# Performance work log

Hardware: AMD Instinct MI355X
Metric: run time of the kernel (lower is better)

## Reference

```python
import jax, jax.numpy as jnp
import numpy as np

B, H, W, C = 16, 64, 64, 256
DIM = 256

def setup_inputs() -> dict:
    key = jax.random.key(0)
    ks = jax.random.split(key, 9)
    s_in = 1.0 / np.sqrt(C)
    x = jax.random.normal(ks[0], (B, H, W, C), dtype=jnp.float32)
    Wq = jax.random.normal(ks[1], (C, DIM), dtype=jnp.float32) * s_in
    bq = jnp.zeros((DIM,), dtype=jnp.float32)
    Wk = jax.random.normal(ks[2], (C, DIM), dtype=jnp.float32) * s_in
    bk = jnp.zeros((DIM,), dtype=jnp.float32)
    Wv = jax.random.normal(ks[3], (C, DIM), dtype=jnp.float32) * s_in
    bv = jnp.zeros((DIM,), dtype=jnp.float32)
    # 'out' conv sees 1 input channel (after the channel reduce_sum)
    Wo = jax.random.normal(ks[4], (1, DIM), dtype=jnp.float32)
    bo = jnp.zeros((DIM,), dtype=jnp.float32)
    return {"x": x, "Wq": Wq, "bq": bq, "Wk": Wk, "bk": bk,
            "Wv": Wv, "bv": bv, "Wo": Wo, "bo": bo}

def reference(x, Wq, bq, Wk, bk, Wv, bv, Wo, bo):
    # 1x1 convs == channel GEMMs
    q = jnp.einsum('bhwc,cd->bhwd', x, Wq) + bq
    k = jnp.einsum('bhwc,cd->bhwd', x, Wk) + bk
    v = jnp.einsum('bhwc,cd->bhwd', x, Wv) + bv
    # channel-reduce score -> [B,H,W,1], softmax jointly over spatial axes
    score = jnp.sum(q * k, axis=-1, keepdims=True)
    attn = jax.nn.softmax(score, axis=(1, 2))
    # channel-reduce of v weighted by per-pixel attn -> [B,H,W,1]
    out = jnp.sum(v * attn, axis=-1, keepdims=True)
    # final 1x1 conv: 1 input channel -> DIM output channels
    return jnp.einsum('bhwc,cd->bhwd', out, Wo) + bo
```

## Files before the change

kernel.cpp:

```cpp
#include <hip/hip_runtime.h>


typedef __bf16 bf16_t;
typedef __attribute__((ext_vector_type(8))) __bf16 bf16x8;
typedef __attribute__((ext_vector_type(4))) __bf16 bf16x4;
typedef __attribute__((ext_vector_type(4))) float f32x4;

#define NBATCH 16
#define CCH    256
#define NPIX   65536
#define PPB    4096

#define MH_OFF    0u
#define ML_OFF    131072u
#define U_OFF     262144u
#define WV_OFF    263168u
#define SCL_OFF   264192u
#define SCORE_OFF 264448u
#define SV_OFF    526592u
#define BMAX_OFF  788736u
#define BSUM_OFF  788800u

__global__ __launch_bounds__(256) void prep_kernel(
    const float* __restrict__ Wq, const float* __restrict__ bq,
    const float* __restrict__ Wk, const float* __restrict__ bk,
    const float* __restrict__ Wv, const float* __restrict__ bv,
    bf16_t* __restrict__ Mh, bf16_t* __restrict__ Ml,
    float* __restrict__ u, float* __restrict__ wv, float* __restrict__ scl)
{
    const int t = threadIdx.x;
    if (blockIdx.x < 256) {
        const int c = blockIdx.x;
        __shared__ __align__(16) float wq_row[256];
        wq_row[t] = Wq[c * 256 + t];
        __syncthreads();
        const float4* wk4 = (const float4*)(Wk + t * 256);
        const float4* wq4 = (const float4*)wq_row;
        float acc = 0.f;
#pragma unroll 8
        for (int i = 0; i < 64; ++i) {
            float4 a = wq4[i], b = wk4[i];
            acc += a.x * b.x + a.y * b.y + a.z * b.z + a.w * b.w;
        }
        bf16_t h = (bf16_t)acc;
        float hf = (float)h;
        bf16_t l = (bf16_t)(acc - hf);
        Mh[c * 256 + t] = h;
        Ml[c * 256 + t] = l;
    } else {
        float uacc = 0.f, wvacc = 0.f;
        const float* wqr = Wq + t * 256;
        const float* wkr = Wk + t * 256;
        const float* wvr = Wv + t * 256;
#pragma unroll 4
        for (int d = 0; d < 256; ++d) {
            uacc += wqr[d] * bk[d] + wkr[d] * bq[d];
            wvacc += wvr[d];
        }
        u[t] = uacc;
        wv[t] = wvacc;
        __shared__ float r1[256], r2[256];
        r1[t] = bq[t] * bk[t];
        r2[t] = bv[t];
        __syncthreads();
        for (int s = 128; s > 0; s >>= 1) {
            if (t < s) { r1[t] += r1[t + s]; r2[t] += r2[t + s]; }
            __syncthreads();
        }
        if (t == 0) { scl[0] = r1[0]; scl[1] = r2[0]; }
    }
}

__global__ __launch_bounds__(256) void score_kernel(
    const float* __restrict__ x,
    const bf16_t* __restrict__ Mh, const bf16_t* __restrict__ Ml,
    const float* __restrict__ u, const float* __restrict__ wvp,
    const float* __restrict__ scl,
    float* __restrict__ score, float* __restrict__ svout)
{
    __shared__ __align__(16) bf16_t Ah[128][72];
    __shared__ __align__(16) bf16_t Al[128][72];
    __shared__ float redS[4][128];
    __shared__ float redV[4][128];

    const int t = threadIdx.x;
    const int lane = t & 63;
    const int wid = t >> 6;
    const int l15 = lane & 15;
    const int lg = lane >> 4;
    const int pix0 = blockIdx.x * 128;
    const int wcol0 = wid * 64;

    f32x4 acc[8][4];
#pragma unroll
    for (int i = 0; i < 8; ++i)
#pragma unroll
        for (int j = 0; j < 4; ++j)
            acc[i][j] = (f32x4){0.f, 0.f, 0.f, 0.f};

    for (int kc = 0; kc < 4; ++kc) {
        const int k0 = kc * 64;
        __syncthreads();
#pragma unroll
        for (int i = 0; i < 8; ++i) {
            int li = i * 256 + t;
            int r = li >> 4;
            int c4 = (li & 15) << 2;
            float4 xv = *(const float4*)(x + (size_t)(pix0 + r) * 256 + k0 + c4);
            bf16x4 hi, lo;
            hi[0] = (bf16_t)xv.x; hi[1] = (bf16_t)xv.y;
            hi[2] = (bf16_t)xv.z; hi[3] = (bf16_t)xv.w;
            lo[0] = (bf16_t)(xv.x - (float)hi[0]);
            lo[1] = (bf16_t)(xv.y - (float)hi[1]);
            lo[2] = (bf16_t)(xv.z - (float)hi[2]);
            lo[3] = (bf16_t)(xv.w - (float)hi[3]);
            *(bf16x4*)&Ah[r][c4] = hi;
            *(bf16x4*)&Al[r][c4] = lo;
        }
        __syncthreads();
#pragma unroll
        for (int seg = 0; seg < 3; ++seg) {
            const bf16_t* Bsrc = (seg == 2) ? Ml : Mh;
#pragma unroll
            for (int ks = 0; ks < 2; ++ks) {
                const int kk = ks * 32;
                bf16x8 af[8];
#pragma unroll
                for (int rf = 0; rf < 8; ++rf) {
                    const bf16_t* ap = (seg == 1) ? &Al[rf * 16 + l15][kk + lg * 8]
                                                  : &Ah[rf * 16 + l15][kk + lg * 8];
                    af[rf] = *(const bf16x8*)ap;
                }
                bf16x8 bfr[4];
#pragma unroll
                for (int cf = 0; cf < 4; ++cf) {
                    int col = wcol0 + cf * 16 + l15;
                    bfr[cf] = *(const bf16x8*)(Bsrc + (size_t)col * 256 + k0 + kk + lg * 8);
                }
#pragma unroll
                for (int rf = 0; rf < 8; ++rf)
#pragma unroll
                    for (int cf = 0; cf < 4; ++cf)
                        acc[rf][cf] = __builtin_amdgcn_mfma_f32_16x16x32_bf16(
                            af[rf], bfr[cf], acc[rf][cf], 0, 0, 0);
            }
        }
    }

    float uu[4], wvl[4];
#pragma unroll
    for (int cf = 0; cf < 4; ++cf) {
        uu[cf] = u[wcol0 + cf * 16 + l15];
        wvl[cf] = wvp[wcol0 + cf * 16 + l15];
    }
#pragma unroll
    for (int rf = 0; rf < 8; ++rf) {
#pragma unroll
        for (int r = 0; r < 4; ++r) {
            int row = rf * 16 + lg * 4 + r;
            const float* xr = x + (size_t)(pix0 + row) * 256 + wcol0 + l15;
            float s = 0.f, v = 0.f;
#pragma unroll
            for (int cf = 0; cf < 4; ++cf) {
                float xv = xr[cf * 16];
                s += xv * (acc[rf][cf][r] + uu[cf]);
                v += xv * wvl[cf];
            }
#pragma unroll
            for (int m = 1; m < 16; m <<= 1) {
                s += __shfl_xor(s, m, 64);
                v += __shfl_xor(v, m, 64);
            }
            if (l15 == 0) { redS[wid][row] = s; redV[wid][row] = v; }
        }
    }
    __syncthreads();
    if (t < 128) {
        float c0 = scl[0], bvs = scl[1];
        float s = redS[0][t] + redS[1][t] + redS[2][t] + redS[3][t] + c0;
        float v = redV[0][t] + redV[1][t] + redV[2][t] + redV[3][t] + bvs;
        score[pix0 + t] = s;
        svout[pix0 + t] = v;
    }
}

__global__ __launch_bounds__(256) void stats_kernel(
    const float* __restrict__ score,
    float* __restrict__ bmax, float* __restrict__ bsum)
{
    const int b = blockIdx.x, t = threadIdx.x;
    const float* s = score + b * PPB;
    __shared__ float red[256];
    float m = -1e30f;
    for (int i = t; i < PPB; i += 256) m = fmaxf(m, s[i]);
    red[t] = m;
    __syncthreads();
    for (int k = 128; k > 0; k >>= 1) {
        if (t < k) red[t] = fmaxf(red[t], red[t + k]);
        __syncthreads();
    }
    m = red[0];
    __syncthreads();
    float sum = 0.f;
    for (int i = t; i < PPB; i += 256) sum += __expf(s[i] - m);
    red[t] = sum;
    __syncthreads();
    for (int k = 128; k > 0; k >>= 1) {
        if (t < k) red[t] += red[t + k];
        __syncthreads();
    }
    if (t == 0) { bmax[b] = m; bsum[b] = red[0]; }
}

__global__ __launch_bounds__(256) void out_kernel(
    const float* __restrict__ score, const float* __restrict__ sv,
    const float* __restrict__ bmax, const float* __restrict__ bsum,
    const float* __restrict__ Wo, const float* __restrict__ bo,
    float* __restrict__ out)
{
    const int total = NPIX * 64;
    const int stride = gridDim.x * blockDim.x;
    for (int idx = blockIdx.x * blockDim.x + threadIdx.x; idx < total; idx += stride) {
        int p = idx >> 6;
        int c4 = (idx & 63) << 2;
        int b = p >> 12;
        float g = __expf(score[p] - bmax[b]) / bsum[b] * sv[p];
        float4 w = *(const float4*)(Wo + c4);
        float4 bb = *(const float4*)(bo + c4);
        float4 o = { g * w.x + bb.x, g * w.y + bb.y, g * w.z + bb.z, g * w.w + bb.w };
        *(float4*)(out + (size_t)p * 256 + c4) = o;
    }
}

extern "C" void kernel_launch(void* const* d_in, const int* in_sizes, int n_in,
                              void* d_out, int out_size, void* d_ws, size_t ws_size,
                              hipStream_t stream) {
    const float* x  = (const float*)d_in[0];
    const float* Wq = (const float*)d_in[1];
    const float* bq = (const float*)d_in[2];
    const float* Wk = (const float*)d_in[3];
    const float* bk = (const float*)d_in[4];
    const float* Wv = (const float*)d_in[5];
    const float* bv = (const float*)d_in[6];
    const float* Wo = (const float*)d_in[7];
    const float* bo = (const float*)d_in[8];
    float* out = (float*)d_out;
    char* ws = (char*)d_ws;

    bf16_t* Mh = (bf16_t*)(ws + MH_OFF);
    bf16_t* Ml = (bf16_t*)(ws + ML_OFF);
    float* u   = (float*)(ws + U_OFF);
    float* wv  = (float*)(ws + WV_OFF);
    float* scl = (float*)(ws + SCL_OFF);
    float* score = (float*)(ws + SCORE_OFF);
    float* sv    = (float*)(ws + SV_OFF);
    float* bmax  = (float*)(ws + BMAX_OFF);
    float* bsum  = (float*)(ws + BSUM_OFF);

    prep_kernel<<<dim3(257), dim3(256), 0, stream>>>(Wq, bq, Wk, bk, Wv, bv, Mh, Ml, u, wv, scl);
    score_kernel<<<dim3(NPIX / 128), dim3(256), 0, stream>>>(x, Mh, Ml, u, wv, scl, score, sv);
    stats_kernel<<<dim3(NBATCH), dim3(256), 0, stream>>>(score, bmax, bsum);
    out_kernel<<<dim3(2048), dim3(256), 0, stream>>>(score, sv, bmax, bsum, Wo, bo, out);
}
```

Measured before the change: 125.8 us.

## Stage full-K x tile in swizzled LDS, halve pixel tile, reuse LDS for epilogue

The score kernel now loads a whole 64-pixel by 256-channel x tile into LDS at once as bf16 hi/lo, using an XOR swizzle instead of padding, rather than looping over four K-chunks with a sync around each. It drops from 128 to 64 pixels per block, doubling the grid and cutting accumulators from 32 to 16 fragments to help fit two blocks per CU. The epilogue rebuilds x from hi+lo in LDS instead of re-reading x from global memory, and the reduction buffers share the same LDS. Each block now uses 64KB of LDS, which caps occupancy, and B fragments are reloaded from global for half as many rows, so weight reuse per load is lower.

```diff
diff --git a/kernel.cpp b/kernel.cpp
--- a/kernel.cpp
+++ b/kernel.cpp
@@ -7,7 +7,6 @@
 typedef __attribute__((ext_vector_type(4))) float f32x4;
 
 #define NBATCH 16
-#define CCH    256
 #define NPIX   65536
 #define PPB    4096
 
@@ -71,80 +70,94 @@
     }
 }
 
-__global__ __launch_bounds__(256) void score_kernel(
+__device__ __forceinline__ int swz(int row, int col) {
+    return row * 256 + (col ^ ((row & 7) << 3));
+}
+
+__global__ __launch_bounds__(256, 2) void score_kernel(
     const float* __restrict__ x,
     const bf16_t* __restrict__ Mh, const bf16_t* __restrict__ Ml,
     const float* __restrict__ u, const float* __restrict__ wvp,
     const float* __restrict__ scl,
     float* __restrict__ score, float* __restrict__ svout)
 {
-    __shared__ __align__(16) bf16_t Ah[128][72];
-    __shared__ __align__(16) bf16_t Al[128][72];
-    __shared__ float redS[4][128];
-    __shared__ float redV[4][128];
+    __shared__ __align__(16) char smem[65536];
+    bf16_t* Ah = (bf16_t*)smem;
+    bf16_t* Al = Ah + 16384;
+    float* redS = (float*)smem;
+    float* redV = redS + 256;
 
     const int t = threadIdx.x;
     const int lane = t & 63;
     const int wid = t >> 6;
     const int l15 = lane & 15;
     const int lg = lane >> 4;
-    const int pix0 = blockIdx.x * 128;
+    const int pix0 = blockIdx.x * 64;
     const int wcol0 = wid * 64;
 
-    f32x4 acc[8][4];
-#pragma unroll
-    for (int i = 0; i < 8; ++i)
+#pragma unroll
+    for (int i = 0; i < 16; ++i) {
+        int chunk = i * 256 + t;
+        int r = chunk >> 6;
+        int c4 = (chunk & 63) << 2;
+        float4 xv = *(const float4*)(x + (size_t)(pix0 + r) * 256 + c4);
+        bf16x4 hi, lo;
+        hi[0] = (bf16_t)xv.x; hi[1] = (bf16_t)xv.y;
+        hi[2] = (bf16_t)xv.z; hi[3] = (bf16_t)xv.w;
+        lo[0] = (bf16_t)(xv.x - (float)hi[0]);
+        lo[1] = (bf16_t)(xv.y - (float)hi[1]);
+        lo[2] = (bf16_t)(xv.z - (float)hi[2]);
+        lo[3] = (bf16_t)(xv.w - (float)hi[3]);
+        int idx = swz(r, c4);
+        *(bf16x4*)&Ah[idx] = hi;
+        *(bf16x4*)&Al[idx] = lo;
+    }
+    __syncthreads();
+
+    f32x4 acc[4][4];
+#pragma unroll
+    for (int i = 0; i < 4; ++i)
 #pragma unroll
         for (int j = 0; j < 4; ++j)
             acc[i][j] = (f32x4){0.f, 0.f, 0.f, 0.f};
 
-    for (int kc = 0; kc < 4; ++kc) {
-        const int k0 = kc * 64;
-        __syncthreads();
-#pragma unroll
-        for (int i = 0; i < 8; ++i) {
-            int li = i * 256 + t;
-            int r = li >> 4;
-            int c4 = (li & 15) << 2;
-            float4 xv = *(const float4*)(x + (size_t)(pix0 + r) * 256 + k0 + c4);
-            bf16x4 hi, lo;
-            hi[0] = (bf16_t)xv.x; hi[1] = (bf16_t)xv.y;
-            hi[2] = (bf16_t)xv.z; hi[3] = (bf16_t)xv.w;
-            lo[0] = (bf16_t)(xv.x - (float)hi[0]);
-            lo[1] = (bf16_t)(xv.y - (float)hi[1]);
-            lo[2] = (bf16_t)(xv.z - (float)hi[2]);
-            lo[3] = (bf16_t)(xv.w - (float)hi[3]);
-            *(bf16x4*)&Ah[r][c4] = hi;
-            *(bf16x4*)&Al[r][c4] = lo;
-        }
-        __syncthreads();
-#pragma unroll
-        for (int seg = 0; seg < 3; ++seg) {
-            const bf16_t* Bsrc = (seg == 2) ? Ml : Mh;
-#pragma unroll
-            for (int ks = 0; ks < 2; ++ks) {
-                const int kk = ks * 32;
-                bf16x8 af[8];
-#pragma unroll
-                for (int rf = 0; rf < 8; ++rf) {
-                    const bf16_t* ap = (seg == 1) ? &Al[rf * 16 + l15][kk + lg * 8]
-                                                  : &Ah[rf * 16 + l15][kk + lg * 8];
-                    af[rf] = *(const bf16x8*)ap;
-                }
-                bf16x8 bfr[4];
-#pragma unroll
-                for (int cf = 0; cf < 4; ++cf) {
-                    int col = wcol0 + cf * 16 + l15;
-                    bfr[cf] = *(const bf16x8*)(Bsrc + (size_t)col * 256 + k0 + kk + lg * 8);
-                }
-#pragma unroll
-                for (int rf = 0; rf < 8; ++rf)
-#pragma unroll
-                    for (int cf = 0; cf < 4; ++cf)
-                        acc[rf][cf] = __builtin_amdgcn_mfma_f32_16x16x32_bf16(
-                            af[rf], bfr[cf], acc[rf][cf], 0, 0, 0);
-            }
-        }
+#pragma unroll
+    for (int ks = 0; ks < 8; ++ks) {
+        const int k0 = ks * 32;
+        bf16x8 af_h[4], af_l[4];
+#pragma unroll
+        for (int rf = 0; rf < 4; ++rf) {
+            int row = rf * 16 + l15;
+            int idx = swz(row, k0 + lg * 8);
+            af_h[rf] = *(const bf16x8*)&Ah[idx];
+            af_l[rf] = *(const bf16x8*)&Al[idx];
+        }
+        bf16x8 bfr_h[4], bfr_l[4];
+#pragma unroll
+        for (int cf = 0; cf < 4; ++cf) {
+            int col = wcol0 + cf * 16 + l15;
+            size_t boff = (size_t)col * 256 + k0 + lg * 8;
+            bfr_h[cf] = *(const bf16x8*)(Mh + boff);
+            bfr_l[cf] = *(const bf16x8*)(Ml + boff);
+        }
+#pragma unroll
+        for (int rf = 0; rf < 4; ++rf)
+#pragma unroll
+            for (int cf = 0; cf < 4; ++cf)
+                acc[rf][cf] = __builtin_amdgcn_mfma_f32_16x16x32_bf16(
+                    af_h[rf], bfr_h[cf], acc[rf][cf], 0, 0, 0);
+#pragma unroll
+        for (int rf = 0; rf < 4; ++rf)
+#pragma unroll
+            for (int cf = 0; cf < 4; ++cf)
+                acc[rf][cf] = __builtin_amdgcn_mfma_f32_16x16x32_bf16(
+                    af_l[rf], bfr_h[cf], acc[rf][cf], 0, 0, 0);
+#pragma unroll
+        for (int rf = 0; rf < 4; ++rf)
+#pragma unroll
+            for (int cf = 0; cf < 4; ++cf)
+                acc[rf][cf] = __builtin_amdgcn_mfma_f32_16x16x32_bf16(
+                    af_h[rf], bfr_l[cf], acc[rf][cf], 0, 0, 0);
     }
 
     float uu[4], wvl[4];
@@ -153,16 +166,18 @@
         uu[cf] = u[wcol0 + cf * 16 + l15];
         wvl[cf] = wvp[wcol0 + cf * 16 + l15];
     }
-#pragma unroll
-    for (int rf = 0; rf < 8; ++rf) {
+    float sacc[4][4], vacc[4][4];
+#pragma unroll
+    for (int rf = 0; rf < 4; ++rf) {
 #pragma unroll
         for (int r = 0; r < 4; ++r) {
             int row = rf * 16 + lg * 4 + r;
-            const float* xr = x + (size_t)(pix0 + row) * 256 + wcol0 + l15;
             float s = 0.f, v = 0.f;
 #pragma unroll
             for (int cf = 0; cf < 4; ++cf) {
-                float xv = xr[cf * 16];
+                int col = wcol0 + cf * 16 + l15;
+                int idx = swz(row, col);
+                float xv = (float)Ah[idx] + (float)Al[idx];
                 s += xv * (acc[rf][cf][r] + uu[cf]);
                 v += xv * wvl[cf];
             }
@@ -171,14 +186,26 @@
                 s += __shfl_xor(s, m, 64);
                 v += __shfl_xor(v, m, 64);
             }
-            if (l15 == 0) { redS[wid][row] = s; redV[wid][row] = v; }
-        }
-    }
-    __syncthreads();
-    if (t < 128) {
+            sacc[rf][r] = s;
+            vacc[rf][r] = v;
+        }
+    }
+    __syncthreads();
+    if (l15 == 0) {
+#pragma unroll
+        for (int rf = 0; rf < 4; ++rf)
+#pragma unroll
+            for (int r = 0; r < 4; ++r) {
+                int row = rf * 16 + lg * 4 + r;
+                redS[wid * 64 + row] = sacc[rf][r];
+                redV[wid * 64 + row] = vacc[rf][r];
+            }
+    }
+    __syncthreads();
+    if (t < 64) {
         float c0 = scl[0], bvs = scl[1];
-        float s = redS[0][t] + redS[1][t] + redS[2][t] + redS[3][t] + c0;
-        float v = redV[0][t] + redV[1][t] + redV[2][t] + redV[3][t] + bvs;
+        float s = redS[t] + redS[64 + t] + redS[128 + t] + redS[192 + t] + c0;
+        float v = redV[t] + redV[64 + t] + redV[128 + t] + redV[192 + t] + bvs;
         score[pix0 + t] = s;
         svout[pix0 + t] = v;
     }
@@ -258,7 +285,7 @@
     float* bsum  = (float*)(ws + BSUM_OFF);
 
     prep_kernel<<<dim3(257), dim3(256), 0, stream>>>(Wq, bq, Wk, bk, Wv, bv, Mh, Ml, u, wv, scl);
-    score_kernel<<<dim3(NPIX / 128), dim3(256), 0, stream>>>(x, Mh, Ml, u, wv, scl, score, sv);
+    score_kernel<<<dim3(NPIX / 64), dim3(256), 0, stream>>>(x, Mh, Ml, u, wv, scl, score, sv);
     stats_kernel<<<dim3(NBATCH), dim3(256), 0, stream>>>(score, bmax, bsum);
     out_kernel<<<dim3(2048), dim3(256), 0, stream>>>(score, sv, bmax, bsum, Wo, bo, out);
 }
```

Result: faster. 102.6 us (-18.4%).
